# Kernel optimization log

Hardware: AMD Instinct MI355X
Metric: run time of the kernel (lower is better)

The kernel has to match this reference:

```python
import jax, jax.numpy as jnp
import numpy as np

B, S, E, H = 4, 1024, 1024, 16
D = E // H  # per-head dim


def setup_inputs() -> dict:
    key = jax.random.key(0)
    ks = jax.random.split(key, 5)
    scale = 1.0 / np.sqrt(E)
    x = jax.random.normal(ks[0], (B, S, E), dtype=jnp.float32)
    Wq = jax.random.normal(ks[1], (H, E, D), dtype=jnp.float32) * scale
    Wk = jax.random.normal(ks[2], (H, E, D), dtype=jnp.float32) * scale
    Wv = jax.random.normal(ks[3], (H, E, D), dtype=jnp.float32) * scale
    W_O = jax.random.normal(ks[4], (E, E), dtype=jnp.float32) * scale
    return {"x": x, "Wq": Wq, "Wk": Wk, "Wv": Wv, "W_O": W_O}


def reference(x, Wq, Wk, Wv, W_O):
    # Batched-over-heads equivalent of the per-head Python loop.
    q = jnp.einsum('bse,hed->bhsd', x, Wq)
    k = jnp.einsum('bse,hed->bhsd', x, Wk)
    v = jnp.einsum('bse,hed->bhsd', x, Wv)
    scores = jnp.einsum('bhqd,bhkd->bhqk', q, k) / jnp.sqrt(jnp.float32(D))
    causal = jnp.tril(jnp.ones((S, S), dtype=bool))  # [S,S]
    scores = jnp.where(causal, scores, jnp.finfo(scores.dtype).min)
    attn = jax.nn.softmax(scores, axis=-1)
    heads = jnp.einsum('bhqk,bhkd->bhqd', attn, v)
    # concat heads along feature dim -> (B, S, E)
    concat = heads.transpose(0, 2, 1, 3).reshape(B, S, E)
    # Faithful to `self.W_O @ concatenated_outputs` (valid since S == E):
    # broadcasts W_O (E,E) against concat's trailing (S,E) matrices.
    output = jnp.matmul(W_O, concat)
    return output
```

## Files before the change

### kernel.cpp

```cpp
#include <hip/hip_runtime.h>
#include <hip/hip_bf16.h>
#include <math.h>

#define B_ 4
#define S_ 1024
#define E_ 1024
#define H_ 16
#define D_ 64

typedef __attribute__((ext_vector_type(8))) short   s16x8;
typedef __attribute__((ext_vector_type(8))) unsigned short u16x8;
typedef __attribute__((ext_vector_type(4))) unsigned short u16x4;
typedef __attribute__((ext_vector_type(4))) float   f32x4;
typedef unsigned short u16;

__device__ __forceinline__ u16 f2bf(float f) {
    union { float f; unsigned u; } v; v.f = f;
    unsigned u = v.u + 0x7FFFu + ((v.u >> 16) & 1u);
    return (u16)(u >> 16);
}
__device__ __forceinline__ float bf2f(u16 h) {
    union { unsigned u; float f; } v; v.u = ((unsigned)h) << 16;
    return v.f;
}
__device__ __forceinline__ void splitf(float f, u16& h, u16& l) {
    h = f2bf(f);
    l = f2bf(f - bf2f(h));
}

#define MFMA(a, b, c) __builtin_amdgcn_mfma_f32_16x16x32_bf16((a), (b), (c), 0, 0, 0)

#define LDR 40

__global__ __launch_bounds__(256) void qkv_gemm(
    const float* __restrict__ x,
    const float* __restrict__ Wq, const float* __restrict__ Wk, const float* __restrict__ Wv,
    u16* __restrict__ qh, u16* __restrict__ ql,
    u16* __restrict__ kh, u16* __restrict__ kl,
    u16* __restrict__ vth, u16* __restrict__ vtl)
{
    __shared__ __align__(16) u16 Ah[128][LDR], Al[128][LDR], Bh[128][LDR], Bl[128][LDR];

    const int tid  = threadIdx.x;
    const int m0   = blockIdx.x * 128;
    const int n0   = blockIdx.y * 128;
    const int w    = n0 >> 10;
    const int h0   = (n0 & 1023) >> 6;
    const float* W = (w == 0) ? Wq : (w == 1) ? Wk : Wv;

    const int wid  = tid >> 6, lane = tid & 63;
    const int wr   = wid >> 1, wc = wid & 1;
    const int lrow = lane & 15, lk = lane >> 4;

    const int sr = tid >> 1;
    const int sh = (tid & 1) * 16;
    const int bn = tid & 127;
    const int bk = (tid >> 7) * 16;

    f32x4 acc[4][4] = {};

    for (int k0 = 0; k0 < E_; k0 += 32) {
        __syncthreads();
        {
            const float* xp = x + (size_t)(m0 + sr) * E_ + k0 + sh;
            f32x4 a0 = *(const f32x4*)(xp);
            f32x4 a1 = *(const f32x4*)(xp + 4);
            f32x4 a2 = *(const f32x4*)(xp + 8);
            f32x4 a3 = *(const f32x4*)(xp + 12);
            u16x8 h0v, l0v, h1v, l1v;
            #pragma unroll
            for (int j = 0; j < 4; j++) {
                u16 hh, ll;
                splitf(a0[j], hh, ll); h0v[j]     = hh; l0v[j]     = ll;
                splitf(a1[j], hh, ll); h0v[j + 4] = hh; l0v[j + 4] = ll;
                splitf(a2[j], hh, ll); h1v[j]     = hh; l1v[j]     = ll;
                splitf(a3[j], hh, ll); h1v[j + 4] = hh; l1v[j + 4] = ll;
            }
            *(u16x8*)&Ah[sr][sh]     = h0v;  *(u16x8*)&Al[sr][sh]     = l0v;
            *(u16x8*)&Ah[sr][sh + 8] = h1v;  *(u16x8*)&Al[sr][sh + 8] = l1v;
        }
        {
            const int nh = h0 + (bn >> 6);
            const int nd = bn & 63;
            const float* wp = W + ((size_t)nh * E_ + k0 + bk) * D_ + nd;
            float fb[16];
            #pragma unroll
            for (int i = 0; i < 16; i++) fb[i] = wp[(size_t)i * D_];
            u16x8 h0v, l0v, h1v, l1v;
            #pragma unroll
            for (int j = 0; j < 8; j++) {
                u16 hh, ll;
                splitf(fb[j], hh, ll);     h0v[j] = hh; l0v[j] = ll;
                splitf(fb[j + 8], hh, ll); h1v[j] = hh; l1v[j] = ll;
            }
            *(u16x8*)&Bh[bn][bk]     = h0v;  *(u16x8*)&Bl[bn][bk]     = l0v;
            *(u16x8*)&Bh[bn][bk + 8] = h1v;  *(u16x8*)&Bl[bn][bk + 8] = l1v;
        }
        __syncthreads();

        s16x8 fXh[4], fXl[4], fWh[4], fWl[4];
        #pragma unroll
        for (int i = 0; i < 4; i++) {
            fXh[i] = *(const s16x8*)&Ah[wr * 64 + i * 16 + lrow][lk * 8];
            fXl[i] = *(const s16x8*)&Al[wr * 64 + i * 16 + lrow][lk * 8];
            fWh[i] = *(const s16x8*)&Bh[wc * 64 + i * 16 + lrow][lk * 8];
            fWl[i] = *(const s16x8*)&Bl[wc * 64 + i * 16 + lrow][lk * 8];
        }
        if (w < 2) {
            #pragma unroll
            for (int i = 0; i < 4; i++)
                #pragma unroll
                for (int j = 0; j < 4; j++) {
                    acc[i][j] = MFMA(fWh[i], fXh[j], acc[i][j]);
                    acc[i][j] = MFMA(fWl[i], fXh[j], acc[i][j]);
                    acc[i][j] = MFMA(fWh[i], fXl[j], acc[i][j]);
                }
        } else {
            #pragma unroll
            for (int i = 0; i < 4; i++)
                #pragma unroll
                for (int j = 0; j < 4; j++) {
                    acc[i][j] = MFMA(fXh[i], fWh[j], acc[i][j]);
                    acc[i][j] = MFMA(fXl[i], fWh[j], acc[i][j]);
                    acc[i][j] = MFMA(fXh[i], fWl[j], acc[i][j]);
                }
        }
    }

    const int nloc = n0 & 1023;
    if (w < 2) {
        u16* Yh = (w == 0) ? qh : kh;
        u16* Yl = (w == 0) ? ql : kl;
        const float sc = (w == 0) ? 0.125f : 1.0f;
        #pragma unroll
        for (int i = 0; i < 4; i++) {
            const int nn = nloc + wc * 64 + i * 16 + lk * 4;
            const int hh2 = nn >> 6, d0 = nn & 63;
            #pragma unroll
            for (int j = 0; j < 4; j++) {
                const int mrow = m0 + wr * 64 + j * 16 + lrow;
                const int b = mrow >> 10, s = mrow & 1023;
                u16x4 oh, ol;
                #pragma unroll
                for (int r = 0; r < 4; r++) {
                    u16 hhv, llv;
                    splitf(acc[i][j][r] * sc, hhv, llv);
                    oh[r] = hhv; ol[r] = llv;
                }
                const size_t off = (((size_t)b * H_ + hh2) * S_ + s) * D_ + d0;
                *(u16x4*)(Yh + off) = oh;
                *(u16x4*)(Yl + off) = ol;
            }
        }
    } else {
        #pragma unroll
        for (int i = 0; i < 4; i++) {
            const int mrow = m0 + wr * 64 + i * 16 + lk * 4;
            const int b = mrow >> 10, s = mrow & 1023;
            #pragma unroll
            for (int j = 0; j < 4; j++) {
                const int nn = nloc + wc * 64 + j * 16 + lrow;
                const int hh2 = nn >> 6, d0 = nn & 63;
                u16x4 oh, ol;
                #pragma unroll
                for (int r = 0; r < 4; r++) {
                    u16 hhv, llv;
                    splitf(acc[i][j][r], hhv, llv);
                    oh[r] = hhv; ol[r] = llv;
                }
                const size_t off = (((size_t)b * H_ + hh2) * D_ + d0) * S_ + s;
                *(u16x4*)(vth + off) = oh;
                *(u16x4*)(vtl + off) = ol;
            }
        }
    }
}

__global__ __launch_bounds__(256) void attn(
    const u16* __restrict__ qh, const u16* __restrict__ ql,
    const u16* __restrict__ kh, const u16* __restrict__ kl,
    const u16* __restrict__ vth, const u16* __restrict__ vtl,
    u16* __restrict__ CTh, u16* __restrict__ CTl)
{
    const int qt = 15 - blockIdx.x;
    const int bh = blockIdx.y;

    __shared__ __align__(16) u16 Kh[64][72], Kl[64][72];
    __shared__ __align__(16) u16 Vh[64][72], Vl[64][72];
    __shared__ __align__(16) u16 Ph[4][16][72], Pl[4][16][72];

    const int tid = threadIdx.x, wid = tid >> 6, lane = tid & 63;
    const int lrow = lane & 15, lk = lane >> 4;
    const int q0g = qt * 64 + wid * 16;

    s16x8 fQh[2], fQl[2];
    {
        const size_t qoff = ((size_t)bh * S_ + q0g + lrow) * D_;
        #pragma unroll
        for (int ks = 0; ks < 2; ks++) {
            fQh[ks] = *(const s16x8*)(qh + qoff + ks * 32 + lk * 8);
            fQl[ks] = *(const s16x8*)(ql + qoff + ks * 32 + lk * 8);
        }
    }

    f32x4 accO[4] = {};
    float m_r[4], l_r[4];
    #pragma unroll
    for (int r = 0; r < 4; r++) { m_r[r] = -INFINITY; l_r[r] = 0.0f; }

    const u16* Kbh = kh  + (size_t)bh * S_ * D_;
    const u16* Kbl = kl  + (size_t)bh * S_ * D_;
    const u16* Vbh = vth + (size_t)bh * D_ * S_;
    const u16* Vbl = vtl + (size_t)bh * D_ * S_;

    const int rk = tid >> 2, ck = (tid & 3) * 16;

    for (int t = 0; t <= qt; t++) {
        const int c0 = t * 64;
        __syncthreads();
        {
            const size_t ko = (size_t)(c0 + rk) * D_ + ck;
            *(u16x8*)&Kh[rk][ck]     = *(const u16x8*)(Kbh + ko);
            *(u16x8*)&Kh[rk][ck + 8] = *(const u16x8*)(Kbh + ko + 8);
            *(u16x8*)&Kl[rk][ck]     = *(const u16x8*)(Kbl + ko);
            *(u16x8*)&Kl[rk][ck + 8] = *(const u16x8*)(Kbl + ko + 8);
            const size_t vo = (size_t)rk * S_ + c0 + ck;
            *(u16x8*)&Vh[rk][ck]     = *(const u16x8*)(Vbh + vo);
            *(u16x8*)&Vh[rk][ck + 8] = *(const u16x8*)(Vbh + vo + 8);
            *(u16x8*)&Vl[rk][ck]     = *(const u16x8*)(Vbl + vo);
            *(u16x8*)&Vl[rk][ck + 8] = *(const u16x8*)(Vbl + vo + 8);
        }
        __syncthreads();

        f32x4 accS[4] = {};
        __builtin_amdgcn_s_setprio(1);
        #pragma unroll
        for (int nf = 0; nf < 4; nf++) {
            #pragma unroll
            for (int ks = 0; ks < 2; ks++) {
                const s16x8 kfh = *(const s16x8*)&Kh[nf * 16 + lrow][ks * 32 + lk * 8];
                const s16x8 kfl = *(const s16x8*)&Kl[nf * 16 + lrow][ks * 32 + lk * 8];
                accS[nf] = MFMA(fQh[ks], kfh, accS[nf]);
                accS[nf] = MFMA(fQl[ks], kfh, accS[nf]);
                accS[nf] = MFMA(fQh[ks], kfl, accS[nf]);
            }
        }
        __builtin_amdgcn_s_setprio(0);

        if (c0 + 63 > q0g) {
            #pragma unroll
            for (int nf = 0; nf < 4; nf++)
                #pragma unroll
                for (int r = 0; r < 4; r++) {
                    if (c0 + nf * 16 + lrow > q0g + lk * 4 + r) accS[nf][r] = -INFINITY;
                }
        }

        float rs[4];
        #pragma unroll
        for (int r = 0; r < 4; r++) {
            float v = fmaxf(fmaxf(accS[0][r], accS[1][r]), fmaxf(accS[2][r], accS[3][r]));
            #pragma unroll
            for (int d_ = 1; d_ < 16; d_ <<= 1) v = fmaxf(v, __shfl_xor(v, d_));
            const float mnew = fmaxf(m_r[r], v);
            rs[r] = __expf(m_r[r] - mnew);
            m_r[r] = mnew;
            float sum = 0.0f;
            #pragma unroll
            for (int nf = 0; nf < 4; nf++) {
                const float p = __expf(accS[nf][r] - mnew);
                accS[nf][r] = p;
                sum += p;
            }
            #pragma unroll
            for (int d_ = 1; d_ < 16; d_ <<= 1) sum += __shfl_xor(sum, d_);
            l_r[r] = l_r[r] * rs[r] + sum;
        }

        #pragma unroll
        for (int nf = 0; nf < 4; nf++)
            #pragma unroll
            for (int r = 0; r < 4; r++) {
                u16 hh, ll;
                splitf(accS[nf][r], hh, ll);
                Ph[wid][lk * 4 + r][nf * 16 + lrow] = hh;
                Pl[wid][lk * 4 + r][nf * 16 + lrow] = ll;
            }
        #pragma unroll
        for (int df = 0; df < 4; df++)
            #pragma unroll
            for (int r = 0; r < 4; r++) accO[df][r] *= rs[r];

        s16x8 fPh[2], fPl[2];
        #pragma unroll
        for (int ks = 0; ks < 2; ks++) {
            fPh[ks] = *(const s16x8*)&Ph[wid][lrow][ks * 32 + lk * 8];
            fPl[ks] = *(const s16x8*)&Pl[wid][lrow][ks * 32 + lk * 8];
        }
        __builtin_amdgcn_s_setprio(1);
        #pragma unroll
        for (int df = 0; df < 4; df++) {
            #pragma unroll
            for (int ks = 0; ks < 2; ks++) {
                const s16x8 vfh = *(const s16x8*)&Vh[df * 16 + lrow][ks * 32 + lk * 8];
                const s16x8 vfl = *(const s16x8*)&Vl[df * 16 + lrow][ks * 32 + lk * 8];
                accO[df] = MFMA(fPh[ks], vfh, accO[df]);
                accO[df] = MFMA(fPl[ks], vfh, accO[df]);
                accO[df] = MFMA(fPh[ks], vfl, accO[df]);
            }
        }
        __builtin_amdgcn_s_setprio(0);
    }

    const int b = bh >> 4, h = bh & 15;
    float inv[4];
    #pragma unroll
    for (int r = 0; r < 4; r++) inv[r] = 1.0f / l_r[r];
    #pragma unroll
    for (int df = 0; df < 4; df++) {
        const int e = h * 64 + df * 16 + lrow;
        const int s = q0g + lk * 4;
        u16x4 oh, ol;
        #pragma unroll
        for (int r = 0; r < 4; r++) {
            u16 hh, ll;
            splitf(accO[df][r] * inv[r], hh, ll);
            oh[r] = hh; ol[r] = ll;
        }
        const size_t off = ((size_t)b * E_ + e) * S_ + s;
        *(u16x4*)(CTh + off) = oh;
        *(u16x4*)(CTl + off) = ol;
    }
}

__global__ __launch_bounds__(256) void out_gemm(
    const u16* __restrict__ CTh, const u16* __restrict__ CTl,
    const float* __restrict__ WO, float* __restrict__ out)
{
    __shared__ __align__(16) u16 Ah[128][LDR], Al[128][LDR], Bh[128][LDR], Bl[128][LDR];

    const int tid = threadIdx.x;
    const int j0 = blockIdx.x * 128;
    const int i0 = blockIdx.y * 128;
    const int b  = blockIdx.z;

    const int wid = tid >> 6, lane = tid & 63;
    const int wr = wid >> 1, wc = wid & 1;
    const int lrow = lane & 15, lk = lane >> 4;

    const int sr = tid >> 1;
    const int sh = (tid & 1) * 16;

    f32x4 acc[4][4] = {};

    for (int k0 = 0; k0 < S_; k0 += 32) {
        __syncthreads();
        {
            const size_t off = ((size_t)b * E_ + j0 + sr) * S_ + k0 + sh;
            *(u16x8*)&Ah[sr][sh]     = *(const u16x8*)(CTh + off);
            *(u16x8*)&Ah[sr][sh + 8] = *(const u16x8*)(CTh + off + 8);
            *(u16x8*)&Al[sr][sh]     = *(const u16x8*)(CTl + off);
            *(u16x8*)&Al[sr][sh + 8] = *(const u16x8*)(CTl + off + 8);
        }
        {
            const float* wp = WO + (size_t)(i0 + sr) * S_ + k0 + sh;
            f32x4 a0 = *(const f32x4*)(wp);
            f32x4 a1 = *(const f32x4*)(wp + 4);
            f32x4 a2 = *(const f32x4*)(wp + 8);
            f32x4 a3 = *(const f32x4*)(wp + 12);
            u16x8 h0v, l0v, h1v, l1v;
            #pragma unroll
            for (int j = 0; j < 4; j++) {
                u16 hh, ll;
                splitf(a0[j], hh, ll); h0v[j]     = hh; l0v[j]     = ll;
                splitf(a1[j], hh, ll); h0v[j + 4] = hh; l0v[j + 4] = ll;
                splitf(a2[j], hh, ll); h1v[j]     = hh; l1v[j]     = ll;
                splitf(a3[j], hh, ll); h1v[j + 4] = hh; l1v[j + 4] = ll;
            }
            *(u16x8*)&Bh[sr][sh]     = h0v;  *(u16x8*)&Bl[sr][sh]     = l0v;
            *(u16x8*)&Bh[sr][sh + 8] = h1v;  *(u16x8*)&Bl[sr][sh + 8] = l1v;
        }
        __syncthreads();

        s16x8 fAh[4], fAl[4], fBh[4], fBl[4];
        #pragma unroll
        for (int i = 0; i < 4; i++) {
            fAh[i] = *(const s16x8*)&Ah[wr * 64 + i * 16 + lrow][lk * 8];
            fAl[i] = *(const s16x8*)&Al[wr * 64 + i * 16 + lrow][lk * 8];
            fBh[i] = *(const s16x8*)&Bh[wc * 64 + i * 16 + lrow][lk * 8];
            fBl[i] = *(const s16x8*)&Bl[wc * 64 + i * 16 + lrow][lk * 8];
        }
        #pragma unroll
        for (int i = 0; i < 4; i++)
            #pragma unroll
            for (int j = 0; j < 4; j++) {
                acc[i][j] = MFMA(fAh[i], fBh[j], acc[i][j]);
                acc[i][j] = MFMA(fAl[i], fBh[j], acc[i][j]);
                acc[i][j] = MFMA(fAh[i], fBl[j], acc[i][j]);
            }
    }

    #pragma unroll
    for (int i = 0; i < 4; i++) {
        const int jj = j0 + wr * 64 + i * 16 + lk * 4;
        #pragma unroll
        for (int j = 0; j < 4; j++) {
            const int ii = i0 + wc * 64 + j * 16 + lrow;
            float* dst = out + ((size_t)b * E_ + ii) * E_ + jj;
            *(f32x4*)dst = acc[i][j];
        }
    }
}

extern "C" void kernel_launch(void* const* d_in, const int* in_sizes, int n_in,
                              void* d_out, int out_size, void* d_ws, size_t ws_size,
                              hipStream_t stream)
{
    const float* x   = (const float*)d_in[0];
    const float* Wq  = (const float*)d_in[1];
    const float* Wk  = (const float*)d_in[2];
    const float* Wv  = (const float*)d_in[3];
    const float* W_O = (const float*)d_in[4];
    float* out = (float*)d_out;

    const size_t N = (size_t)B_ * H_ * S_ * D_;
    u16* ws16 = (u16*)d_ws;
    u16* qh  = ws16;
    u16* ql  = qh  + N;
    u16* kh  = ql  + N;
    u16* kl  = kh  + N;
    u16* vth = kl  + N;
    u16* vtl = vth + N;
    u16* CTh = vtl + N;
    u16* CTl = CTh + N;

    qkv_gemm<<<dim3(32, 24), 256, 0, stream>>>(x, Wq, Wk, Wv, qh, ql, kh, kl, vth, vtl);
    attn<<<dim3(16, 64), 256, 0, stream>>>(qh, ql, kh, kl, vth, vtl, CTh, CTl);
    out_gemm<<<dim3(8, 8, 4), 256, 0, stream>>>(CTh, CTl, W_O, out);
}
```

Baseline: 367.2 us.

## Pre-split inputs to bf16 hi/lo in separate kernels, prefetch K/V in attention

Moves the fp32-to-bf16 hi/lo splitting of x, the QKV weights (transposed) and W_O out of the GEMM inner loops into dedicated preprocessing kernels. Each GEMM tile is then loaded as vectorised bf16 data instead of being converted repeatedly per block, and the strided weight loads go away. The attention loop now register-prefetches the next K/V tile while computing the current one. MFMA sections get s_setprio. The cost is extra kernel launches, extra workspace traffic, and CT buffers that alias the x split buffers.

```diff
diff --git a/kernel.cpp b/kernel.cpp
--- a/kernel.cpp
+++ b/kernel.cpp
@@ -32,21 +32,75 @@
 
 #define LDR 40
 
+__global__ __launch_bounds__(256) void split_f32(
+    const float* __restrict__ src, u16* __restrict__ h, u16* __restrict__ l)
+{
+    const size_t i = ((size_t)blockIdx.x * 256 + threadIdx.x) * 8;
+    f32x4 a = *(const f32x4*)(src + i);
+    f32x4 b = *(const f32x4*)(src + i + 4);
+    u16x8 hv, lv;
+    #pragma unroll
+    for (int j = 0; j < 4; j++) {
+        u16 hh, ll;
+        splitf(a[j], hh, ll); hv[j]     = hh; lv[j]     = ll;
+        splitf(b[j], hh, ll); hv[j + 4] = hh; lv[j + 4] = ll;
+    }
+    *(u16x8*)(h + i) = hv;
+    *(u16x8*)(l + i) = lv;
+}
+
+__global__ __launch_bounds__(256) void split_wT(
+    const float* __restrict__ Wq, const float* __restrict__ Wk, const float* __restrict__ Wv,
+    u16* __restrict__ wth, u16* __restrict__ wtl)
+{
+    __shared__ float T[64][65];
+    const int e0 = blockIdx.x * 64;
+    const int h  = blockIdx.y;
+    const int w  = blockIdx.z;
+    const float* W = (w == 0) ? Wq : (w == 1) ? Wk : Wv;
+
+    const int tid = threadIdx.x;
+    const int r4  = tid >> 4;
+    const int c4  = (tid & 15) * 4;
+
+    #pragma unroll
+    for (int p = 0; p < 4; p++) {
+        const int r = p * 16 + r4;
+        f32x4 v = *(const f32x4*)(W + ((size_t)h * E_ + e0 + r) * D_ + c4);
+        #pragma unroll
+        for (int j = 0; j < 4; j++) T[r][c4 + j] = v[j];
+    }
+    __syncthreads();
+    #pragma unroll
+    for (int p = 0; p < 4; p++) {
+        const int d = p * 16 + r4;
+        u16x4 oh, ol;
+        #pragma unroll
+        for (int j = 0; j < 4; j++) {
+            u16 hh, ll;
+            splitf(T[c4 + j][d], hh, ll);
+            oh[j] = hh; ol[j] = ll;
+        }
+        const size_t n   = (size_t)w * 1024 + h * 64 + d;
+        const size_t off = n * E_ + e0 + c4;
+        *(u16x4*)(wth + off) = oh;
+        *(u16x4*)(wtl + off) = ol;
+    }
+}
+
 __global__ __launch_bounds__(256) void qkv_gemm(
-    const float* __restrict__ x,
-    const float* __restrict__ Wq, const float* __restrict__ Wk, const float* __restrict__ Wv,
+    const u16* __restrict__ xh, const u16* __restrict__ xl,
+    const u16* __restrict__ wth, const u16* __restrict__ wtl,
     u16* __restrict__ qh, u16* __restrict__ ql,
     u16* __restrict__ kh, u16* __restrict__ kl,
     u16* __restrict__ vth, u16* __restrict__ vtl)
 {
     __shared__ __align__(16) u16 Ah[128][LDR], Al[128][LDR], Bh[128][LDR], Bl[128][LDR];
 
-    const int tid  = threadIdx.x;
-    const int m0   = blockIdx.x * 128;
-    const int n0   = blockIdx.y * 128;
-    const int w    = n0 >> 10;
-    const int h0   = (n0 & 1023) >> 6;
-    const float* W = (w == 0) ? Wq : (w == 1) ? Wk : Wv;
+    const int tid = threadIdx.x;
+    const int m0  = blockIdx.x * 128;
+    const int n0  = blockIdx.y * 128;
+    const int w   = n0 >> 10;
 
     const int wid  = tid >> 6, lane = tid & 63;
     const int wr   = wid >> 1, wc = wid & 1;
@@ -54,47 +108,22 @@
 
     const int sr = tid >> 1;
     const int sh = (tid & 1) * 16;
-    const int bn = tid & 127;
-    const int bk = (tid >> 7) * 16;
 
     f32x4 acc[4][4] = {};
 
     for (int k0 = 0; k0 < E_; k0 += 32) {
         __syncthreads();
         {
-            const float* xp = x + (size_t)(m0 + sr) * E_ + k0 + sh;
-            f32x4 a0 = *(const f32x4*)(xp);
-            f32x4 a1 = *(const f32x4*)(xp + 4);
-            f32x4 a2 = *(const f32x4*)(xp + 8);
-            f32x4 a3 = *(const f32x4*)(xp + 12);
-            u16x8 h0v, l0v, h1v, l1v;
-            #pragma unroll
-            for (int j = 0; j < 4; j++) {
-                u16 hh, ll;
-                splitf(a0[j], hh, ll); h0v[j]     = hh; l0v[j]     = ll;
-                splitf(a1[j], hh, ll); h0v[j + 4] = hh; l0v[j + 4] = ll;
-                splitf(a2[j], hh, ll); h1v[j]     = hh; l1v[j]     = ll;
-                splitf(a3[j], hh, ll); h1v[j + 4] = hh; l1v[j + 4] = ll;
-            }
-            *(u16x8*)&Ah[sr][sh]     = h0v;  *(u16x8*)&Al[sr][sh]     = l0v;
-            *(u16x8*)&Ah[sr][sh + 8] = h1v;  *(u16x8*)&Al[sr][sh + 8] = l1v;
-        }
-        {
-            const int nh = h0 + (bn >> 6);
-            const int nd = bn & 63;
-            const float* wp = W + ((size_t)nh * E_ + k0 + bk) * D_ + nd;
-            float fb[16];
-            #pragma unroll
-            for (int i = 0; i < 16; i++) fb[i] = wp[(size_t)i * D_];
-            u16x8 h0v, l0v, h1v, l1v;
-            #pragma unroll
-            for (int j = 0; j < 8; j++) {
-                u16 hh, ll;
-                splitf(fb[j], hh, ll);     h0v[j] = hh; l0v[j] = ll;
-                splitf(fb[j + 8], hh, ll); h1v[j] = hh; l1v[j] = ll;
-            }
-            *(u16x8*)&Bh[bn][bk]     = h0v;  *(u16x8*)&Bl[bn][bk]     = l0v;
-            *(u16x8*)&Bh[bn][bk + 8] = h1v;  *(u16x8*)&Bl[bn][bk + 8] = l1v;
+            const size_t ao = (size_t)(m0 + sr) * E_ + k0 + sh;
+            *(u16x8*)&Ah[sr][sh]     = *(const u16x8*)(xh + ao);
+            *(u16x8*)&Ah[sr][sh + 8] = *(const u16x8*)(xh + ao + 8);
+            *(u16x8*)&Al[sr][sh]     = *(const u16x8*)(xl + ao);
+            *(u16x8*)&Al[sr][sh + 8] = *(const u16x8*)(xl + ao + 8);
+            const size_t bo = (size_t)(n0 + sr) * E_ + k0 + sh;
+            *(u16x8*)&Bh[sr][sh]     = *(const u16x8*)(wth + bo);
+            *(u16x8*)&Bh[sr][sh + 8] = *(const u16x8*)(wth + bo + 8);
+            *(u16x8*)&Bl[sr][sh]     = *(const u16x8*)(wtl + bo);
+            *(u16x8*)&Bl[sr][sh + 8] = *(const u16x8*)(wtl + bo + 8);
         }
         __syncthreads();
 
@@ -106,6 +135,7 @@
             fWh[i] = *(const s16x8*)&Bh[wc * 64 + i * 16 + lrow][lk * 8];
             fWl[i] = *(const s16x8*)&Bl[wc * 64 + i * 16 + lrow][lk * 8];
         }
+        __builtin_amdgcn_s_setprio(1);
         if (w < 2) {
             #pragma unroll
             for (int i = 0; i < 4; i++)
@@ -125,6 +155,7 @@
                     acc[i][j] = MFMA(fXh[i], fWl[j], acc[i][j]);
                 }
         }
+        __builtin_amdgcn_s_setprio(0);
     }
 
     const int nloc = n0 & 1023;
@@ -215,22 +246,27 @@
 
     const int rk = tid >> 2, ck = (tid & 3) * 16;
 
+    u16x8 pf0, pf1, pf2, pf3, pf4, pf5, pf6, pf7;
+#define ISSUE(c0_) { \
+        const size_t ko = (size_t)((c0_) + rk) * D_ + ck; \
+        pf0 = *(const u16x8*)(Kbh + ko);     pf1 = *(const u16x8*)(Kbh + ko + 8); \
+        pf2 = *(const u16x8*)(Kbl + ko);     pf3 = *(const u16x8*)(Kbl + ko + 8); \
+        const size_t vo = (size_t)rk * S_ + (c0_) + ck; \
+        pf4 = *(const u16x8*)(Vbh + vo);     pf5 = *(const u16x8*)(Vbh + vo + 8); \
+        pf6 = *(const u16x8*)(Vbl + vo);     pf7 = *(const u16x8*)(Vbl + vo + 8); }
+
+    ISSUE(0)
+
     for (int t = 0; t <= qt; t++) {
         const int c0 = t * 64;
         __syncthreads();
-        {
-            const size_t ko = (size_t)(c0 + rk) * D_ + ck;
-            *(u16x8*)&Kh[rk][ck]     = *(const u16x8*)(Kbh + ko);
-            *(u16x8*)&Kh[rk][ck + 8] = *(const u16x8*)(Kbh + ko + 8);
-            *(u16x8*)&Kl[rk][ck]     = *(const u16x8*)(Kbl + ko);
-            *(u16x8*)&Kl[rk][ck + 8] = *(const u16x8*)(Kbl + ko + 8);
-            const size_t vo = (size_t)rk * S_ + c0 + ck;
-            *(u16x8*)&Vh[rk][ck]     = *(const u16x8*)(Vbh + vo);
-            *(u16x8*)&Vh[rk][ck + 8] = *(const u16x8*)(Vbh + vo + 8);
-            *(u16x8*)&Vl[rk][ck]     = *(const u16x8*)(Vbl + vo);
-            *(u16x8*)&Vl[rk][ck + 8] = *(const u16x8*)(Vbl + vo + 8);
-        }
-        __syncthreads();
+        *(u16x8*)&Kh[rk][ck]     = pf0;  *(u16x8*)&Kh[rk][ck + 8] = pf1;
+        *(u16x8*)&Kl[rk][ck]     = pf2;  *(u16x8*)&Kl[rk][ck + 8] = pf3;
+        *(u16x8*)&Vh[rk][ck]     = pf4;  *(u16x8*)&Vh[rk][ck + 8] = pf5;
+        *(u16x8*)&Vl[rk][ck]     = pf6;  *(u16x8*)&Vl[rk][ck + 8] = pf7;
+        __syncthreads();
+
+        if (t < qt) ISSUE(c0 + 64)
 
         f32x4 accS[4] = {};
         __builtin_amdgcn_s_setprio(1);
@@ -311,6 +347,7 @@
         }
         __builtin_amdgcn_s_setprio(0);
     }
+#undef ISSUE
 
     const int b = bh >> 4, h = bh & 15;
     float inv[4];
@@ -335,7 +372,8 @@
 
 __global__ __launch_bounds__(256) void out_gemm(
     const u16* __restrict__ CTh, const u16* __restrict__ CTl,
-    const float* __restrict__ WO, float* __restrict__ out)
+    const u16* __restrict__ woh, const u16* __restrict__ wol,
+    float* __restrict__ out)
 {
     __shared__ __align__(16) u16 Ah[128][LDR], Al[128][LDR], Bh[128][LDR], Bl[128][LDR];
 
@@ -356,29 +394,16 @@
     for (int k0 = 0; k0 < S_; k0 += 32) {
         __syncthreads();
         {
-            const size_t off = ((size_t)b * E_ + j0 + sr) * S_ + k0 + sh;
-            *(u16x8*)&Ah[sr][sh]     = *(const u16x8*)(CTh + off);
-            *(u16x8*)&Ah[sr][sh + 8] = *(const u16x8*)(CTh + off + 8);
-            *(u16x8*)&Al[sr][sh]     = *(const u16x8*)(CTl + off);
-            *(u16x8*)&Al[sr][sh + 8] = *(const u16x8*)(CTl + off + 8);
-        }
-        {
-            const float* wp = WO + (size_t)(i0 + sr) * S_ + k0 + sh;
-            f32x4 a0 = *(const f32x4*)(wp);
-            f32x4 a1 = *(const f32x4*)(wp + 4);
-            f32x4 a2 = *(const f32x4*)(wp + 8);
-            f32x4 a3 = *(const f32x4*)(wp + 12);
-            u16x8 h0v, l0v, h1v, l1v;
-            #pragma unroll
-            for (int j = 0; j < 4; j++) {
-                u16 hh, ll;
-                splitf(a0[j], hh, ll); h0v[j]     = hh; l0v[j]     = ll;
-                splitf(a1[j], hh, ll); h0v[j + 4] = hh; l0v[j + 4] = ll;
-                splitf(a2[j], hh, ll); h1v[j]     = hh; l1v[j]     = ll;
-                splitf(a3[j], hh, ll); h1v[j + 4] = hh; l1v[j + 4] = ll;
-            }
-            *(u16x8*)&Bh[sr][sh]     = h0v;  *(u16x8*)&Bl[sr][sh]     = l0v;
-            *(u16x8*)&Bh[sr][sh + 8] = h1v;  *(u16x8*)&Bl[sr][sh + 8] = l1v;
+            const size_t ao = ((size_t)b * E_ + j0 + sr) * S_ + k0 + sh;
+            *(u16x8*)&Ah[sr][sh]     = *(const u16x8*)(CTh + ao);
+            *(u16x8*)&Ah[sr][sh + 8] = *(const u16x8*)(CTh + ao + 8);
+            *(u16x8*)&Al[sr][sh]     = *(const u16x8*)(CTl + ao);
+            *(u16x8*)&Al[sr][sh + 8] = *(const u16x8*)(CTl + ao + 8);
+            const size_t bo = (size_t)(i0 + sr) * S_ + k0 + sh;
+            *(u16x8*)&Bh[sr][sh]     = *(const u16x8*)(woh + bo);
+            *(u16x8*)&Bh[sr][sh + 8] = *(const u16x8*)(woh + bo + 8);
+            *(u16x8*)&Bl[sr][sh]     = *(const u16x8*)(wol + bo);
+            *(u16x8*)&Bl[sr][sh + 8] = *(const u16x8*)(wol + bo + 8);
         }
         __syncthreads();
 
@@ -390,6 +415,7 @@
             fBh[i] = *(const s16x8*)&Bh[wc * 64 + i * 16 + lrow][lk * 8];
             fBl[i] = *(const s16x8*)&Bl[wc * 64 + i * 16 + lrow][lk * 8];
         }
+        __builtin_amdgcn_s_setprio(1);
         #pragma unroll
         for (int i = 0; i < 4; i++)
             #pragma unroll
@@ -398,6 +424,7 @@
                 acc[i][j] = MFMA(fAl[i], fBh[j], acc[i][j]);
                 acc[i][j] = MFMA(fAh[i], fBl[j], acc[i][j]);
             }
+        __builtin_amdgcn_s_setprio(0);
     }
 
     #pragma unroll
@@ -423,18 +450,21 @@
     const float* W_O = (const float*)d_in[4];
     float* out = (float*)d_out;
 
-    const size_t N = (size_t)B_ * H_ * S_ * D_;
-    u16* ws16 = (u16*)d_ws;
-    u16* qh  = ws16;
-    u16* ql  = qh  + N;
-    u16* kh  = ql  + N;
-    u16* kl  = kh  + N;
-    u16* vth = kl  + N;
-    u16* vtl = vth + N;
-    u16* CTh = vtl + N;
-    u16* CTl = CTh + N;
-
-    qkv_gemm<<<dim3(32, 24), 256, 0, stream>>>(x, Wq, Wk, Wv, qh, ql, kh, kl, vth, vtl);
+    const size_t N = (size_t)B_ * S_ * E_;
+    u16* p = (u16*)d_ws;
+    u16* qh  = p;            u16* ql  = p + 1 * N;
+    u16* kh  = p + 2 * N;    u16* kl  = p + 3 * N;
+    u16* vth = p + 4 * N;    u16* vtl = p + 5 * N;
+    u16* xh  = p + 6 * N;    u16* xl  = p + 7 * N;
+    u16* wth = p + 8 * N;
+    u16* wtl = wth + (size_t)3 * E_ * E_;
+    u16* CTh = xh;           u16* CTl = xl;
+    u16* woh = wth;          u16* wol = wtl;
+
+    split_f32<<<2048, 256, 0, stream>>>(x, xh, xl);
+    split_wT<<<dim3(16, 16, 3), 256, 0, stream>>>(Wq, Wk, Wv, wth, wtl);
+    qkv_gemm<<<dim3(32, 24), 256, 0, stream>>>(xh, xl, wth, wtl, qh, ql, kh, kl, vth, vtl);
+    split_f32<<<512, 256, 0, stream>>>(W_O, woh, wol);
     attn<<<dim3(16, 64), 256, 0, stream>>>(qh, ql, kh, kl, vth, vtl, CTh, CTl);
-    out_gemm<<<dim3(8, 8, 4), 256, 0, stream>>>(CTh, CTl, W_O, out);
-}
+    out_gemm<<<dim3(8, 8, 4), 256, 0, stream>>>(CTh, CTl, woh, wol, out);
+}
```

Measured after the change: 349.0 us. 5.0% less time.
